# Performance work log

Measured on AMD Instinct MI355X. Metric: run time of the kernel, lower is better.

Reference implementation:

```python
import jax, jax.numpy as jnp
import numpy as np
from jax import lax

# Dimensions (see shape_source)
B, J, I, E, H = 256, 128, 64, 512, 512   # batch, target len, source len, embed, hidden
MAXJW = 128                               # max jump width
WJ = 2 * MAXJW + 1                        # size of jump-width set (257)
ALPHA_P0 = 1.0
EPS = 1e-29


def setup_inputs() -> dict:
    key = jax.random.key(0)
    ks = jax.random.split(key, 10)
    return {
        "y_hidden": jax.random.normal(ks[0], (B, J, E), jnp.float32),
        "y_hidden_null": jax.random.normal(ks[1], (1, 1, E), jnp.float32),
        "W_trans": jax.random.normal(ks[2], (E, H), jnp.float32) * 0.02,
        "b_trans": jnp.zeros((H,), jnp.float32),
        "W_jump": jax.random.normal(ks[3], (H, WJ), jnp.float32) * 0.02,
        "b_jump": jnp.zeros((WJ,), jnp.float32),
        "W_p0": jax.random.normal(ks[4], (H, 1), jnp.float32) * 0.02,
        "b_p0": jnp.zeros((1,), jnp.float32),
        # emission probs p(source_t | target_state_k), kept near 1 to avoid
        # underflow of the unrescaled HMM forward product (as in original).
        "emission": jax.random.uniform(ks[5], (B, 2 * J, I), jnp.float32) * 0.5 + 0.75,
        "source_lengths": jax.random.randint(ks[6], (B,), 1, I + 1, dtype=jnp.int32),
        "target_lengths": jax.random.randint(ks[7], (B,), 1, J + 1, dtype=jnp.int32),
    }


def _build_transition(y_hidden, y_hidden_null, W_trans, b_trans, W_jump, b_jump, W_p0, b_p0):
    # get_transition: Dense(tanh) -> Dense(softmax) jump widths; Dense(sigmoid) p0.
    ts = jnp.tanh(y_hidden @ W_trans + b_trans)           # [B,J,H]
    ts_null = jnp.tanh(y_hidden_null @ W_trans + b_trans) # [1,1,H]
    jump_prob = jax.nn.softmax(ts @ W_jump + b_jump, axis=-1)  # [B,J,WJ]
    p0_scalar = ALPHA_P0 * jax.nn.sigmoid(ts_null @ W_p0 + b_p0)[0, 0, 0]
    p0 = jnp.broadcast_to(p0_scalar, (y_hidden.shape[0], J))  # tile to [B,J]
    # gather jump widths: row i takes jump_prob[:, i, MAXJW + k - i] for k in [0,J)
    idx = MAXJW + jnp.arange(J)[None, :] - jnp.arange(J)[:, None]        # [J,J]
    idxb = jnp.broadcast_to(idx[None], (jump_prob.shape[0], J, J))
    jw = jnp.take_along_axis(jump_prob, idxb, axis=2)                    # [B,J,J]
    jw = jw * (1.0 - p0[:, :, None]) / jnp.sum(jw, axis=2, keepdims=True)
    diag_p0 = p0[:, :, None] * jnp.eye(J, dtype=jw.dtype)                # [B,J,J]
    T_half = jnp.concatenate([jw, diag_p0], axis=2)                      # [B,J,2J]
    return jnp.concatenate([T_half, T_half], axis=1)                     # [B,2J,2J]


def reference(y_hidden, y_hidden_null, W_trans, b_trans, W_jump, b_jump,
              W_p0, b_p0, emission, source_lengths, target_lengths):
    T = _build_transition(y_hidden, y_hidden_null, W_trans, b_trans,
                          W_jump, b_jump, W_p0, b_p0)       # [B,2J,2J]
    e = jnp.transpose(emission, (2, 0, 1))                  # [I,B,2J]
    # tf.scan with no initializer: f_0 = emission at source position 0
    f0 = e[0]

    def step(f, et):
        f_next = jnp.einsum('bj,bjk->bk', f, T) * et        # forward recursion
        return f_next, f_next

    _, fs = lax.scan(step, f0, e[1:])
    fs = jnp.concatenate([f0[None], fs], axis=0)            # [I,B,2J]
    fbt = jnp.transpose(fs, (1, 2, 0))                      # [B,2J,I]
    last_idx = (source_lengths - 1).astype(jnp.int32)[:, None, None]
    last = jnp.take_along_axis(fbt, last_idx, axis=2)[:, :, 0]  # [B,2J]
    m = (jnp.arange(J)[None, :] < target_lengths[:, None]).astype(last.dtype)
    mask = jnp.concatenate([m, m], axis=1)                  # [B,2J]
    return jnp.log(jnp.sum(last * mask, axis=1) + EPS)      # [B]
```

## Files before the change

kernel.cpp:

```cpp
#include <hip/hip_runtime.h>
#include <stdint.h>

typedef __attribute__((ext_vector_type(8))) short bf16x8;
typedef __attribute__((ext_vector_type(4))) float f32x4;

__device__ __forceinline__ unsigned short f2bf(float f) {
  union { float f; unsigned int u; } un; un.f = f;
  unsigned int r = un.u + 0x7fffu + ((un.u >> 16) & 1u);
  return (unsigned short)(r >> 16);
}

__device__ __forceinline__ float bf2f(unsigned short u) {
  union { unsigned int u; float f; } un; un.u = ((unsigned int)u) << 16;
  return un.f;
}

__device__ __forceinline__ float tanh_fast(float x) {
  x = fminf(15.f, fmaxf(-15.f, x));
  float e = __expf(2.f * x);
  return (e - 1.f) / (e + 1.f);
}

__device__ __forceinline__ unsigned int cvt_pk_bf16(float lo, float hi) {
  unsigned int r;
  asm("v_cvt_pk_bf16_f32 %0, %1, %2" : "=v"(r) : "v"(lo), "v"(hi));
  return r;
}

__device__ __forceinline__ void gload_lds16(const void* g, void* l) {
  __builtin_amdgcn_global_load_lds(
      (const __attribute__((address_space(1))) unsigned int*)(unsigned long long)g,
      (__attribute__((address_space(3))) unsigned int*)(unsigned int)(unsigned long long)l,
      16, 0, 0);
}

__global__ __launch_bounds__(256) void cvt_weights(
    const float* __restrict__ Wt_in, const float* __restrict__ Wj_in,
    unsigned short* __restrict__ wt, unsigned short* __restrict__ wj) {
  const int i = blockIdx.x * 256 + threadIdx.x;
  if (i < 512 * 512) {
    const int c = i >> 9, r = i & 511;
    wt[i] = f2bf(Wt_in[(size_t)r * 512 + c]);
  } else {
    const int j = i - 512 * 512;
    const int c = j >> 9, r = j & 511;
    wj[j] = f2bf(Wj_in[(size_t)r * 257 + c]);
  }
}

__global__ __launch_bounds__(512) void p0_kernel(
    const float* __restrict__ ynull, const float* __restrict__ W_trans,
    const float* __restrict__ b_trans, const float* __restrict__ W_p0,
    const float* __restrict__ b_p0, float* __restrict__ p0buf) {
  __shared__ float red[512];
  const int hh = threadIdx.x;
  float acc = 0.f;
  for (int e = 0; e < 512; ++e) acc = fmaf(ynull[e], W_trans[(size_t)e * 512 + hh], acc);
  const float ts = tanhf(acc + b_trans[hh]);
  red[hh] = ts * W_p0[hh];
  __syncthreads();
  for (int s = 256; s > 0; s >>= 1) {
    if (hh < s) red[hh] += red[hh + s];
    __syncthreads();
  }
  if (hh == 0) {
    const float z = red[0] + b_p0[0];
    const float p0 = 1.f / (1.f + __expf(-z));
    p0buf[0] = p0;
    p0buf[1] = 1.f - p0;
  }
}


__global__ __launch_bounds__(256, 2) void gemm_af32(
    const float* __restrict__ A, const unsigned short* __restrict__ Bt,
    const float* __restrict__ bias, unsigned short* __restrict__ Cout,
    int M, int N, int K) {
  __shared__ unsigned short sA[128 * 32];
  __shared__ unsigned short sB[128 * 32];
  const int tid = threadIdx.x;
  const int lane = tid & 63;
  const int wave = tid >> 6;
  const int wr = wave >> 1, wc = wave & 1;
  const int m0 = blockIdx.x * 128, n0 = blockIdx.y * 128;

  f32x4 acc[4][4] = {};

  const int srow = lane >> 2;
  const int sl = lane & 3;
  const int scol = sl * 8;
  const int wsz = (srow >> 1) & 3;
  const int scolw = (sl ^ wsz) * 8;
  const int c0 = wave * 2, c1 = wave * 2 + 1;
  const float* Af0 = A + (size_t)(m0 + c0 * 16 + srow) * K + scol;
  const float* Af1 = A + (size_t)(m0 + c1 * 16 + srow) * K + scol;
  const unsigned short* Br0 = Bt + (size_t)(n0 + c0 * 16 + srow) * K + scolw;
  const unsigned short* Br1 = Bt + (size_t)(n0 + c1 * 16 + srow) * K + scolw;

  float4 a00 = *reinterpret_cast<const float4*>(Af0);
  float4 a01 = *reinterpret_cast<const float4*>(Af0 + 4);
  float4 a10 = *reinterpret_cast<const float4*>(Af1);
  float4 a11 = *reinterpret_cast<const float4*>(Af1 + 4);

  const int r15 = lane & 15;
  const int oslot = ((lane >> 4) ^ ((r15 >> 1) & 3)) * 8;

  for (int kk = 0; kk < K; kk += 32) {
    __syncthreads();
    {
      union { unsigned int u[4]; bf16x8 v; } p;
      p.u[0] = cvt_pk_bf16(a00.x, a00.y);
      p.u[1] = cvt_pk_bf16(a00.z, a00.w);
      p.u[2] = cvt_pk_bf16(a01.x, a01.y);
      p.u[3] = cvt_pk_bf16(a01.z, a01.w);
      *reinterpret_cast<bf16x8*>(&sA[c0 * 512 + srow * 32 + scolw]) = p.v;
      p.u[0] = cvt_pk_bf16(a10.x, a10.y);
      p.u[1] = cvt_pk_bf16(a10.z, a10.w);
      p.u[2] = cvt_pk_bf16(a11.x, a11.y);
      p.u[3] = cvt_pk_bf16(a11.z, a11.w);
      *reinterpret_cast<bf16x8*>(&sA[c1 * 512 + srow * 32 + scolw]) = p.v;
    }
    gload_lds16(Br0 + kk, &sB[c0 * 512]);
    gload_lds16(Br1 + kk, &sB[c1 * 512]);
    __syncthreads();
    if (kk + 32 < K) {
      a00 = *reinterpret_cast<const float4*>(Af0 + kk + 32);
      a01 = *reinterpret_cast<const float4*>(Af0 + kk + 36);
      a10 = *reinterpret_cast<const float4*>(Af1 + kk + 32);
      a11 = *reinterpret_cast<const float4*>(Af1 + kk + 36);
    }
    bf16x8 af[4], bfr[4];
#pragma unroll
    for (int mi = 0; mi < 4; ++mi)
      af[mi] = *reinterpret_cast<const bf16x8*>(
          &sA[(wr * 64 + mi * 16 + r15) * 32 + oslot]);
#pragma unroll
    for (int ni = 0; ni < 4; ++ni)
      bfr[ni] = *reinterpret_cast<const bf16x8*>(
          &sB[(wc * 64 + ni * 16 + r15) * 32 + oslot]);
#pragma unroll
    for (int mi = 0; mi < 4; ++mi)
#pragma unroll
      for (int ni = 0; ni < 4; ++ni)
        acc[mi][ni] = __builtin_amdgcn_mfma_f32_16x16x32_bf16(
            af[mi], bfr[ni], acc[mi][ni], 0, 0, 0);
  }

  const int crow0 = m0 + wr * 64 + (lane >> 4) * 4;
  const int ccol0 = n0 + wc * 64 + r15;
#pragma unroll
  for (int mi = 0; mi < 4; ++mi) {
#pragma unroll
    for (int ni = 0; ni < 4; ++ni) {
      const int gcol = ccol0 + ni * 16;
      const float bv = bias[gcol];
#pragma unroll
      for (int r = 0; r < 4; ++r) {
        const int grow = crow0 + mi * 16 + r;
        Cout[(size_t)grow * N + gcol] = f2bf(tanh_fast(acc[mi][ni][r] + bv));
      }
    }
  }
}

__global__ __launch_bounds__(256, 2) void gemm_tt(
    const unsigned short* __restrict__ A, const unsigned short* __restrict__ Bt,
    const float* __restrict__ bias, unsigned short* __restrict__ Cout,
    int M, int N, int K) {
  __shared__ unsigned short sA[128 * 32];
  __shared__ unsigned short sB[128 * 32];
  const int tid = threadIdx.x;
  const int lane = tid & 63;
  const int wave = tid >> 6;
  const int wr = wave >> 1, wc = wave & 1;
  const int m0 = blockIdx.x * 128, n0 = blockIdx.y * 128;

  f32x4 acc[4][4] = {};

  const int srow = lane >> 2;
  const int sl = lane & 3;
  const int wsz = (srow >> 1) & 3;
  const int scolw = (sl ^ wsz) * 8;
  const int c0 = wave * 2, c1 = wave * 2 + 1;
  const unsigned short* Ar0 = A + (size_t)(m0 + c0 * 16 + srow) * K + scolw;
  const unsigned short* Ar1 = A + (size_t)(m0 + c1 * 16 + srow) * K + scolw;
  const unsigned short* Br0 = Bt + (size_t)(n0 + c0 * 16 + srow) * K + scolw;
  const unsigned short* Br1 = Bt + (size_t)(n0 + c1 * 16 + srow) * K + scolw;

  const int r15 = lane & 15;
  const int oslot = ((lane >> 4) ^ ((r15 >> 1) & 3)) * 8;

  for (int kk = 0; kk < K; kk += 32) {
    __syncthreads();
    gload_lds16(Ar0 + kk, &sA[c0 * 512]);
    gload_lds16(Ar1 + kk, &sA[c1 * 512]);
    gload_lds16(Br0 + kk, &sB[c0 * 512]);
    gload_lds16(Br1 + kk, &sB[c1 * 512]);
    __syncthreads();
    bf16x8 af[4], bfr[4];
#pragma unroll
    for (int mi = 0; mi < 4; ++mi)
      af[mi] = *reinterpret_cast<const bf16x8*>(
          &sA[(wr * 64 + mi * 16 + r15) * 32 + oslot]);
#pragma unroll
    for (int ni = 0; ni < 4; ++ni)
      bfr[ni] = *reinterpret_cast<const bf16x8*>(
          &sB[(wc * 64 + ni * 16 + r15) * 32 + oslot]);
#pragma unroll
    for (int mi = 0; mi < 4; ++mi)
#pragma unroll
      for (int ni = 0; ni < 4; ++ni)
        acc[mi][ni] = __builtin_amdgcn_mfma_f32_16x16x32_bf16(
            af[mi], bfr[ni], acc[mi][ni], 0, 0, 0);
  }

  const int crow0 = m0 + wr * 64 + (lane >> 4) * 4;
  const int ccol0 = n0 + wc * 64 + r15;
#pragma unroll
  for (int mi = 0; mi < 4; ++mi) {
#pragma unroll
    for (int ni = 0; ni < 4; ++ni) {
      const int gcol = ccol0 + ni * 16;
      const float bv = bias[gcol];
#pragma unroll
      for (int r = 0; r < 4; ++r) {
        const int grow = crow0 + mi * 16 + r;
        Cout[(size_t)grow * N + gcol] = f2bf(acc[mi][ni][r] + bv);
      }
    }
  }
}

__global__ __launch_bounds__(256) void wsoftmax_kernel(
    const unsigned short* __restrict__ logits, const float* __restrict__ p0buf,
    unsigned short* __restrict__ jwout) {
  const int lane = threadIdx.x & 63;
  const int wave = threadIdx.x >> 6;
  const int row = blockIdx.x * 4 + wave;
  const int i = row & 127;
  const unsigned short* lrow = logits + (size_t)row * 256 + (128 - i);
  const float v0 = bf2f(lrow[lane]);
  const float v1 = bf2f(lrow[lane + 64]);
  float mx = fmaxf(v0, v1);
#pragma unroll
  for (int off = 32; off > 0; off >>= 1) mx = fmaxf(mx, __shfl_xor(mx, off));
  const float e0 = __expf(v0 - mx);
  const float e1 = __expf(v1 - mx);
  float s = e0 + e1;
#pragma unroll
  for (int off = 32; off > 0; off >>= 1) s += __shfl_xor(s, off);
  const float scale = p0buf[1] / s;
  unsigned short* orow = jwout + (size_t)row * 128;
  orow[lane] = f2bf(e0 * scale);
  orow[lane + 64] = f2bf(e1 * scale);
}

#define SE_STRIDE 264
__global__ __launch_bounds__(256, 1) void forward_fused(
    const unsigned short* __restrict__ jwb,
    const float* __restrict__ emission,
    const float* __restrict__ p0buf, const int* __restrict__ slen_p,
    const int* __restrict__ tlen_p, float* __restrict__ out) {
  __shared__ __align__(16) float se[64 * SE_STRIDE];
  __shared__ __align__(16) unsigned short gl16[128];
  const int b = blockIdx.x;
  const int tid = threadIdx.x;
  const float* eb = emission + (size_t)b * 16384;

  bf16x8 bfr[4][8];
  const int l = tid & 63;
  const int m = l & 15;
  const int q = l >> 4;

  if (tid >= 64) {
#pragma unroll
    for (int it = 0; it < 6; ++it) {
      const int tau = (tid - 64) + 192 * it;
      if (tau < 1024) {
        const int t0 = (tau & 15) * 4;
        const int mm = (tau >> 4) & 15;
        const int nt0 = ((tau >> 8) & 1) * 4;
        const int half = (tau >> 9) & 1;
        const int kbase = half * 128 + nt0 * 16 + mm;
        const float4 v0 = *reinterpret_cast<const float4*>(&eb[(size_t)(kbase) * 64 + t0]);
        const float4 v1 = *reinterpret_cast<const float4*>(&eb[(size_t)(kbase + 16) * 64 + t0]);
        const float4 v2 = *reinterpret_cast<const float4*>(&eb[(size_t)(kbase + 32) * 64 + t0]);
        const float4 v3 = *reinterpret_cast<const float4*>(&eb[(size_t)(kbase + 48) * 64 + t0]);
        const int jinv0 = half * 128 + mm * 8 + nt0;
        float* d = &se[(size_t)t0 * SE_STRIDE + jinv0];
        *reinterpret_cast<float4*>(d) = (float4){v0.x, v1.x, v2.x, v3.x};
        *reinterpret_cast<float4*>(d + SE_STRIDE) = (float4){v0.y, v1.y, v2.y, v3.y};
        *reinterpret_cast<float4*>(d + 2 * SE_STRIDE) = (float4){v0.z, v1.z, v2.z, v3.z};
        *reinterpret_cast<float4*>(d + 3 * SE_STRIDE) = (float4){v0.w, v1.w, v2.w, v3.w};
      }
    }
  } else {
    const unsigned short* jwt = jwb + (size_t)b * 16384;
#pragma unroll
    for (int kt = 0; kt < 4; ++kt) {
      const int r0 = kt * 32 + q * 8;
#pragma unroll
      for (int nt = 0; nt < 8; ++nt) {
        const int c = nt * 16 + m;
        bf16x8 v;
#pragma unroll
        for (int j = 0; j < 8; ++j) v[j] = (short)jwt[(size_t)(r0 + j) * 128 + c];
        bfr[kt][nt] = v;
      }
    }
  }
  __syncthreads();
  if (tid >= 64) return;

  const float p0 = p0buf[0];
  const int S = slen_p[b];
  const int T = tlen_p[b];

  float gown[8];
  {
    const float4 i0a = *reinterpret_cast<const float4*>(&se[m * 8]);
    const float4 i0b = *reinterpret_cast<const float4*>(&se[m * 8 + 4]);
    const float4 i1a = *reinterpret_cast<const float4*>(&se[128 + m * 8]);
    const float4 i1b = *reinterpret_cast<const float4*>(&se[128 + m * 8 + 4]);
    gown[0] = i0a.x + i1a.x; gown[1] = i0a.y + i1a.y;
    gown[2] = i0a.z + i1a.z; gown[3] = i0a.w + i1a.w;
    gown[4] = i0b.x + i1b.x; gown[5] = i0b.y + i1b.y;
    gown[6] = i0b.z + i1b.z; gown[7] = i0b.w + i1b.w;
  }
  gl16[(2 * q) * 16 + m]     = f2bf(gown[2 * q]);
  gl16[(2 * q + 1) * 16 + m] = f2bf(gown[2 * q + 1]);

  for (int t = 1; t < S; ++t) {
    const float* st = &se[(size_t)t * SE_STRIDE];
    const float4 pe0a = *reinterpret_cast<const float4*>(&st[m * 8]);
    const float4 pe0b = *reinterpret_cast<const float4*>(&st[m * 8 + 4]);
    const float4 pe1a = *reinterpret_cast<const float4*>(&st[128 + m * 8]);
    const float4 pe1b = *reinterpret_cast<const float4*>(&st[128 + m * 8 + 4]);
    const float e0[8] = {pe0a.x, pe0a.y, pe0a.z, pe0a.w, pe0b.x, pe0b.y, pe0b.z, pe0b.w};
    const float e1[8] = {pe1a.x, pe1a.y, pe1a.z, pe1a.w, pe1b.x, pe1b.y, pe1b.z, pe1b.w};
    float h[8];
#pragma unroll
    for (int nt = 0; nt < 8; ++nt) h[nt] = gown[nt] * (p0 * e1[nt]);
    bf16x8 af[4];
#pragma unroll
    for (int kt = 0; kt < 4; ++kt)
      af[kt] = *reinterpret_cast<const bf16x8*>(&gl16[kt * 32 + q * 8]);
    f32x4 acc[8];
#pragma unroll
    for (int nt = 0; nt < 8; ++nt) {
      f32x4 a = __builtin_amdgcn_mfma_f32_16x16x32_bf16(
          af[0], bfr[0][nt], (f32x4){0.f, 0.f, 0.f, 0.f}, 0, 0, 0);
      a = __builtin_amdgcn_mfma_f32_16x16x32_bf16(af[1], bfr[1][nt], a, 0, 0, 0);
      a = __builtin_amdgcn_mfma_f32_16x16x32_bf16(af[2], bfr[2][nt], a, 0, 0, 0);
      acc[nt] = __builtin_amdgcn_mfma_f32_16x16x32_bf16(af[3], bfr[3][nt], a, 0, 0, 0);
    }
#pragma unroll
    for (int nt = 0; nt < 8; ++nt) gown[nt] = fmaf(acc[nt][0], e0[nt], h[nt]);
    gl16[(2 * q) * 16 + m]     = f2bf(gown[2 * q]);
    gl16[(2 * q + 1) * 16 + m] = f2bf(gown[2 * q + 1]);
  }

  float val = 0.f;
#pragma unroll
  for (int nt = 0; nt < 8; ++nt)
    if (nt * 16 + m < T) val += gown[nt];
#pragma unroll
  for (int off = 1; off < 16; off <<= 1) val += __shfl_xor(val, off);
  if (l == 0) out[b] = logf(val + 1e-29f);
}

extern "C" void kernel_launch(void* const* d_in, const int* in_sizes, int n_in,
                              void* d_out, int out_size, void* d_ws, size_t ws_size,
                              hipStream_t stream) {
  const float* y_hidden = (const float*)d_in[0];
  const float* y_null   = (const float*)d_in[1];
  const float* W_trans  = (const float*)d_in[2];
  const float* b_trans  = (const float*)d_in[3];
  const float* W_jump   = (const float*)d_in[4];
  const float* b_jump   = (const float*)d_in[5];
  const float* W_p0     = (const float*)d_in[6];
  const float* b_p0     = (const float*)d_in[7];
  const float* emission = (const float*)d_in[8];
  const int* slen = (const int*)d_in[9];
  const int* tlen = (const int*)d_in[10];
  float* out = (float*)d_out;

  char* ws = (char*)d_ws;
  unsigned short* ts16  = (unsigned short*)ws;
  unsigned short* lg16  = (unsigned short*)(ws + 33554432);
  unsigned short* wt16t = (unsigned short*)(ws + 50331648);
  unsigned short* wj16t = (unsigned short*)(ws + 50855936);
  float* p0buf          = (float*)(ws + 51118080);
  unsigned short* jwb16 = (unsigned short*)(ws + 51118336);

  cvt_weights<<<dim3(1536), dim3(256), 0, stream>>>(W_trans, W_jump, wt16t, wj16t);
  p0_kernel<<<dim3(1), dim3(512), 0, stream>>>(y_null, W_trans, b_trans, W_p0, b_p0, p0buf);

  gemm_af32<<<dim3(256, 4), dim3(256), 0, stream>>>(y_hidden, wt16t, b_trans, ts16,
                                                    32768, 512, 512);
  gemm_tt<<<dim3(256, 2), dim3(256), 0, stream>>>(ts16, wj16t, b_jump, lg16,
                                                  32768, 256, 512);
  wsoftmax_kernel<<<dim3(8192), dim3(256), 0, stream>>>(lg16, p0buf, jwb16);
  forward_fused<<<dim3(256), dim3(256), 0, stream>>>(jwb16, emission, p0buf,
                                                     slen, tlen, out);
}
```

Measured before the change: 115.7 us.

## Double-buffer GEMM LDS tiles, remap blocks per XCD, merge p0 into weight conversion

```diff
diff --git a/kernel.cpp b/kernel.cpp
--- a/kernel.cpp
+++ b/kernel.cpp
@@ -34,32 +34,36 @@
       16, 0, 0);
 }
 
-__global__ __launch_bounds__(256) void cvt_weights(
+__global__ __launch_bounds__(256) void cvt_weights_p0(
     const float* __restrict__ Wt_in, const float* __restrict__ Wj_in,
-    unsigned short* __restrict__ wt, unsigned short* __restrict__ wj) {
-  const int i = blockIdx.x * 256 + threadIdx.x;
-  if (i < 512 * 512) {
-    const int c = i >> 9, r = i & 511;
-    wt[i] = f2bf(Wt_in[(size_t)r * 512 + c]);
-  } else {
-    const int j = i - 512 * 512;
-    const int c = j >> 9, r = j & 511;
-    wj[j] = f2bf(Wj_in[(size_t)r * 257 + c]);
-  }
-}
-
-__global__ __launch_bounds__(512) void p0_kernel(
-    const float* __restrict__ ynull, const float* __restrict__ W_trans,
-    const float* __restrict__ b_trans, const float* __restrict__ W_p0,
-    const float* __restrict__ b_p0, float* __restrict__ p0buf) {
-  __shared__ float red[512];
+    const float* __restrict__ ynull, const float* __restrict__ b_trans,
+    const float* __restrict__ W_p0, const float* __restrict__ b_p0,
+    unsigned short* __restrict__ wt, unsigned short* __restrict__ wj,
+    float* __restrict__ p0buf) {
+  if (blockIdx.x < 1536) {
+    const int i = blockIdx.x * 256 + threadIdx.x;
+    if (i < 512 * 512) {
+      const int c = i >> 9, r = i & 511;
+      wt[i] = f2bf(Wt_in[(size_t)r * 512 + c]);
+    } else {
+      const int j = i - 512 * 512;
+      const int c = j >> 9, r = j & 511;
+      wj[j] = f2bf(Wj_in[(size_t)r * 257 + c]);
+    }
+    return;
+  }
+  __shared__ float red[256];
   const int hh = threadIdx.x;
-  float acc = 0.f;
-  for (int e = 0; e < 512; ++e) acc = fmaf(ynull[e], W_trans[(size_t)e * 512 + hh], acc);
-  const float ts = tanhf(acc + b_trans[hh]);
-  red[hh] = ts * W_p0[hh];
+  float a0 = 0.f, a1 = 0.f;
+  for (int e = 0; e < 512; ++e) {
+    const float y = ynull[e];
+    a0 = fmaf(y, Wt_in[(size_t)e * 512 + hh], a0);
+    a1 = fmaf(y, Wt_in[(size_t)e * 512 + hh + 256], a1);
+  }
+  red[hh] = tanhf(a0 + b_trans[hh]) * W_p0[hh] +
+            tanhf(a1 + b_trans[hh + 256]) * W_p0[hh + 256];
   __syncthreads();
-  for (int s = 256; s > 0; s >>= 1) {
+  for (int s = 128; s > 0; s >>= 1) {
     if (hh < s) red[hh] += red[hh + s];
     __syncthreads();
   }
@@ -77,12 +81,15 @@
     const float* __restrict__ bias, unsigned short* __restrict__ Cout,
     int M, int N, int K) {
   __shared__ unsigned short sA[128 * 32];
-  __shared__ unsigned short sB[128 * 32];
+  __shared__ unsigned short sB[2][128 * 32];
   const int tid = threadIdx.x;
   const int lane = tid & 63;
   const int wave = tid >> 6;
   const int wr = wave >> 1, wc = wave & 1;
-  const int m0 = blockIdx.x * 128, n0 = blockIdx.y * 128;
+  const int id = blockIdx.x;
+  const int xcd = id & 7, qq = id >> 3;
+  const int m0 = (xcd * 32 + (qq >> 2)) * 128;
+  const int n0 = (qq & 3) * 128;
 
   f32x4 acc[4][4] = {};
 
@@ -97,16 +104,19 @@
   const unsigned short* Br0 = Bt + (size_t)(n0 + c0 * 16 + srow) * K + scolw;
   const unsigned short* Br1 = Bt + (size_t)(n0 + c1 * 16 + srow) * K + scolw;
 
+  const int r15 = lane & 15;
+  const int oslot = ((lane >> 4) ^ ((r15 >> 1) & 3)) * 8;
+  const int nt = K >> 5;
+
   float4 a00 = *reinterpret_cast<const float4*>(Af0);
   float4 a01 = *reinterpret_cast<const float4*>(Af0 + 4);
   float4 a10 = *reinterpret_cast<const float4*>(Af1);
   float4 a11 = *reinterpret_cast<const float4*>(Af1 + 4);
-
-  const int r15 = lane & 15;
-  const int oslot = ((lane >> 4) ^ ((r15 >> 1) & 3)) * 8;
-
-  for (int kk = 0; kk < K; kk += 32) {
-    __syncthreads();
+  gload_lds16(Br0, &sB[0][c0 * 512]);
+  gload_lds16(Br1, &sB[0][c1 * 512]);
+  __syncthreads();
+
+  for (int t = 0; t < nt; ++t) {
     {
       union { unsigned int u[4]; bf16x8 v; } p;
       p.u[0] = cvt_pk_bf16(a00.x, a00.y);
@@ -120,14 +130,14 @@
       p.u[3] = cvt_pk_bf16(a11.z, a11.w);
       *reinterpret_cast<bf16x8*>(&sA[c1 * 512 + srow * 32 + scolw]) = p.v;
     }
-    gload_lds16(Br0 + kk, &sB[c0 * 512]);
-    gload_lds16(Br1 + kk, &sB[c1 * 512]);
     __syncthreads();
-    if (kk + 32 < K) {
-      a00 = *reinterpret_cast<const float4*>(Af0 + kk + 32);
-      a01 = *reinterpret_cast<const float4*>(Af0 + kk + 36);
-      a10 = *reinterpret_cast<const float4*>(Af1 + kk + 32);
-      a11 = *reinterpret_cast<const float4*>(Af1 + kk + 36);
+    if (t + 1 < nt) {
+      gload_lds16(Br0 + (t + 1) * 32, &sB[(t + 1) & 1][c0 * 512]);
+      gload_lds16(Br1 + (t + 1) * 32, &sB[(t + 1) & 1][c1 * 512]);
+      a00 = *reinterpret_cast<const float4*>(Af0 + (t + 1) * 32);
+      a01 = *reinterpret_cast<const float4*>(Af0 + (t + 1) * 32 + 4);
+      a10 = *reinterpret_cast<const float4*>(Af1 + (t + 1) * 32);
+      a11 = *reinterpret_cast<const float4*>(Af1 + (t + 1) * 32 + 4);
     }
     bf16x8 af[4], bfr[4];
 #pragma unroll
@@ -137,13 +147,14 @@
 #pragma unroll
     for (int ni = 0; ni < 4; ++ni)
       bfr[ni] = *reinterpret_cast<const bf16x8*>(
-          &sB[(wc * 64 + ni * 16 + r15) * 32 + oslot]);
+          &sB[t & 1][(wc * 64 + ni * 16 + r15) * 32 + oslot]);
 #pragma unroll
     for (int mi = 0; mi < 4; ++mi)
 #pragma unroll
       for (int ni = 0; ni < 4; ++ni)
         acc[mi][ni] = __builtin_amdgcn_mfma_f32_16x16x32_bf16(
             af[mi], bfr[ni], acc[mi][ni], 0, 0, 0);
+    __syncthreads();
   }
 
   const int crow0 = m0 + wr * 64 + (lane >> 4) * 4;
@@ -167,13 +178,16 @@
     const unsigned short* __restrict__ A, const unsigned short* __restrict__ Bt,
     const float* __restrict__ bias, unsigned short* __restrict__ Cout,
     int M, int N, int K) {
-  __shared__ unsigned short sA[128 * 32];
-  __shared__ unsigned short sB[128 * 32];
+  __shared__ unsigned short sA[2][128 * 32];
+  __shared__ unsigned short sB[2][128 * 32];
   const int tid = threadIdx.x;
   const int lane = tid & 63;
   const int wave = tid >> 6;
   const int wr = wave >> 1, wc = wave & 1;
-  const int m0 = blockIdx.x * 128, n0 = blockIdx.y * 128;
+  const int id = blockIdx.x;
+  const int xcd = id & 7, qq = id >> 3;
+  const int m0 = (xcd * 32 + (qq >> 1)) * 128;
+  const int n0 = (qq & 1) * 128;
 
   f32x4 acc[4][4] = {};
 
@@ -189,29 +203,35 @@
 
   const int r15 = lane & 15;
   const int oslot = ((lane >> 4) ^ ((r15 >> 1) & 3)) * 8;
-
-  for (int kk = 0; kk < K; kk += 32) {
-    __syncthreads();
-    gload_lds16(Ar0 + kk, &sA[c0 * 512]);
-    gload_lds16(Ar1 + kk, &sA[c1 * 512]);
-    gload_lds16(Br0 + kk, &sB[c0 * 512]);
-    gload_lds16(Br1 + kk, &sB[c1 * 512]);
-    __syncthreads();
+  const int nt = K >> 5;
+
+  auto stage = [&](int bi, int t) {
+    gload_lds16(Ar0 + t * 32, &sA[bi][c0 * 512]);
+    gload_lds16(Ar1 + t * 32, &sA[bi][c1 * 512]);
+    gload_lds16(Br0 + t * 32, &sB[bi][c0 * 512]);
+    gload_lds16(Br1 + t * 32, &sB[bi][c1 * 512]);
+  };
+
+  stage(0, 0);
+  __syncthreads();
+  for (int t = 0; t < nt; ++t) {
+    if (t + 1 < nt) stage((t + 1) & 1, t + 1);
     bf16x8 af[4], bfr[4];
 #pragma unroll
     for (int mi = 0; mi < 4; ++mi)
       af[mi] = *reinterpret_cast<const bf16x8*>(
-          &sA[(wr * 64 + mi * 16 + r15) * 32 + oslot]);
+          &sA[t & 1][(wr * 64 + mi * 16 + r15) * 32 + oslot]);
 #pragma unroll
     for (int ni = 0; ni < 4; ++ni)
       bfr[ni] = *reinterpret_cast<const bf16x8*>(
-          &sB[(wc * 64 + ni * 16 + r15) * 32 + oslot]);
+          &sB[t & 1][(wc * 64 + ni * 16 + r15) * 32 + oslot]);
 #pragma unroll
     for (int mi = 0; mi < 4; ++mi)
 #pragma unroll
       for (int ni = 0; ni < 4; ++ni)
         acc[mi][ni] = __builtin_amdgcn_mfma_f32_16x16x32_bf16(
             af[mi], bfr[ni], acc[mi][ni], 0, 0, 0);
+    __syncthreads();
   }
 
   const int crow0 = m0 + wr * 64 + (lane >> 4) * 4;
@@ -393,13 +413,13 @@
   float* p0buf          = (float*)(ws + 51118080);
   unsigned short* jwb16 = (unsigned short*)(ws + 51118336);
 
-  cvt_weights<<<dim3(1536), dim3(256), 0, stream>>>(W_trans, W_jump, wt16t, wj16t);
-  p0_kernel<<<dim3(1), dim3(512), 0, stream>>>(y_null, W_trans, b_trans, W_p0, b_p0, p0buf);
-
-  gemm_af32<<<dim3(256, 4), dim3(256), 0, stream>>>(y_hidden, wt16t, b_trans, ts16,
-                                                    32768, 512, 512);
-  gemm_tt<<<dim3(256, 2), dim3(256), 0, stream>>>(ts16, wj16t, b_jump, lg16,
-                                                  32768, 256, 512);
+  cvt_weights_p0<<<dim3(1537), dim3(256), 0, stream>>>(
+      W_trans, W_jump, y_null, b_trans, W_p0, b_p0, wt16t, wj16t, p0buf);
+
+  gemm_af32<<<dim3(1024), dim3(256), 0, stream>>>(y_hidden, wt16t, b_trans, ts16,
+                                                  32768, 512, 512);
+  gemm_tt<<<dim3(512), dim3(256), 0, stream>>>(ts16, wj16t, b_jump, lg16,
+                                               32768, 256, 512);
   wsoftmax_kernel<<<dim3(8192), dim3(256), 0, stream>>>(lg16, p0buf, jwb16);
   forward_fused<<<dim3(256), dim3(256), 0, stream>>>(jwb16, emission, p0buf,
                                                      slen, tlen, out);
```

Measured after the change: 114.6 us. No clear change (-1.0%).
